# Performance work log

Hardware: AMD Instinct MI355X
Metric: run time of the kernel (lower is better)

The kernel has to match this reference:

```python
import jax, jax.numpy as jnp
import numpy as np

N_NODES = 50000
N_EDGES = 1_600_000
IN_CH = 128
HEADS = 4
OUT_CH = 16
NEG_SLOPE = 0.2


def setup_inputs() -> dict:
    key = jax.random.key(0)
    ks = jax.random.split(key, 6)
    x = jax.random.normal(ks[0], (N_NODES, IN_CH), dtype=jnp.float32)
    row = jax.random.randint(ks[1], (N_EDGES,), 0, N_NODES, dtype=jnp.int32)
    # offset in [1, N) guarantees no self loops in the input graph
    off = jax.random.randint(ks[2], (N_EDGES,), 1, N_NODES, dtype=jnp.int32)
    col = (row + off) % N_NODES
    edge_index = jnp.stack([row, col], axis=0)  # [2, E]
    edge_attr = jax.random.uniform(ks[3], (N_EDGES, HEADS), dtype=jnp.float32)
    weight = jax.random.normal(ks[4], (IN_CH, HEADS * OUT_CH), dtype=jnp.float32) * (1.0 / np.sqrt(IN_CH))
    att_weight = jax.random.normal(ks[5], (1, HEADS, 2 * OUT_CH), dtype=jnp.float32) * 0.1
    bias = jnp.zeros((HEADS * OUT_CH,), dtype=jnp.float32)
    return {"x": x, "edge_index": edge_index, "edge_attr": edge_attr,
            "weight": weight, "att_weight": att_weight, "bias": bias}


def reference(x, edge_index, edge_attr, weight, att_weight, bias):
    N = x.shape[0]
    H, C = HEADS, OUT_CH
    # linear projection: [N, in] @ [in, H*C] -> [N, H, C]
    h = (x @ weight).reshape(N, H, C)
    # add self loops (input is guaranteed self-loop free); self-loop edge_attr = 1
    loop = jnp.arange(N, dtype=edge_index.dtype)
    row = jnp.concatenate([edge_index[0], loop])
    col = jnp.concatenate([edge_index[1], loop])
    ea = jnp.concatenate([edge_attr, jnp.ones((N, H), dtype=edge_attr.dtype)], axis=0)
    edge_index_full = jnp.stack([row, col], axis=0)
    # attention score: cat([h[row], h[col]], -1) * att_weight, summed over feature dim
    a_src = att_weight[0, :, :C]   # [H, C]
    a_dst = att_weight[0, :, C:]   # [H, C]
    alpha = (jnp.einsum('ehc,hc->eh', h[row], a_src)
             + jnp.einsum('ehc,hc->eh', h[col], a_dst))  # [E+N, H]
    alpha = jnp.where(alpha >= 0, alpha, NEG_SLOPE * alpha)  # leaky_relu
    alpha = alpha * ea
    # weighted aggregation: scatter-add messages to row nodes
    msg = alpha[:, :, None] * h[col]                 # [E+N, H, C]
    out = jax.ops.segment_sum(msg, row, num_segments=N)  # [N, H, C]
    out = out.reshape(N, H * C) + bias               # concat heads
    return (out, edge_index_full, alpha)
```

## Files before the change

### kernel.cpp

```cpp
#include <hip/hip_runtime.h>

#define N_NODES 50000
#define N_EDGES 1600000
#define IN_CH 128
#define HEADS 4
#define HC 64
#define E_FULL (N_EDGES + N_NODES)
#define NEG_SLOPE 0.2f

#define BUCKET_NODES 98
#define NBUCK 512
#define BIN_TILE 2048
#define NBLK_BIN ((N_EDGES + BIN_TILE - 1) / BIN_TILE)
#define T_FLAT (NBUCK * NBLK_BIN)
#define SCANA_BLOCKS (T_FLAT / 256)

typedef __attribute__((ext_vector_type(8))) short short8v;
typedef __attribute__((ext_vector_type(4))) float float4v;

__device__ __forceinline__ float leaky(float s) { return s >= 0.f ? s : NEG_SLOPE * s; }

__device__ __forceinline__ unsigned f2bf(float f) {
    unsigned u = __float_as_uint(f);
    return (u + 0x7fffu + ((u >> 16) & 1u)) >> 16;
}
__device__ __forceinline__ float bf2f(unsigned v) {
    return __uint_as_float(v << 16);
}

__global__ __launch_bounds__(256) void wcvt_kernel(
    const float* __restrict__ w, unsigned short* __restrict__ wT)
{
    int i = blockIdx.x * 256 + threadIdx.x;
    if (i < IN_CH * HC) {
        int k = i >> 6, c = i & 63;
        wT[c * IN_CH + k] = (unsigned short)f2bf(w[i]);
    }
}

__global__ __launch_bounds__(256) void gemm_h_kernel(
    const float* __restrict__ x, const unsigned short* __restrict__ wT,
    const float* __restrict__ att, unsigned short* __restrict__ h16,
    float* __restrict__ s_src, float* __restrict__ s_dst)
{
    __shared__ unsigned short x_lds[64 * 128];
    const int tid = threadIdx.x;
    const int nbase = blockIdx.x * 64;

    #pragma unroll
    for (int s = 0; s < 8; ++s) {
        int i = s * 256 + tid;
        int node = i >> 5;
        int q = i & 31;
        float4 v = make_float4(0.f, 0.f, 0.f, 0.f);
        int gn = nbase + node;
        if (gn < N_NODES) v = ((const float4*)x)[(size_t)gn * 32 + q];
        ushort4 b;
        b.x = (unsigned short)f2bf(v.x);
        b.y = (unsigned short)f2bf(v.y);
        b.z = (unsigned short)f2bf(v.z);
        b.w = (unsigned short)f2bf(v.w);
        int chunk = q >> 1, half = q & 1;
        int sw = chunk ^ (node & 7);
        *(ushort4*)&x_lds[node * 128 + sw * 8 + half * 4] = b;
    }
    __syncthreads();

    const int wid = tid >> 6, lane = tid & 63;
    const int g = lane >> 4, m = lane & 15;
    const int rt = wid;

    float4v acc[4] = {{0.f,0.f,0.f,0.f},{0.f,0.f,0.f,0.f},
                      {0.f,0.f,0.f,0.f},{0.f,0.f,0.f,0.f}};
    #pragma unroll
    for (int kk = 0; kk < 4; ++kk) {
        int chunk = (kk * 4 + g) ^ (m & 7);
        short8v a = *(const short8v*)&x_lds[(rt * 16 + m) * 128 + chunk * 8];
        #pragma unroll
        for (int ct = 0; ct < 4; ++ct) {
            short8v bfr = *(const short8v*)&wT[(ct * 16 + m) * IN_CH + kk * 32 + g * 8];
            acc[ct] = __builtin_amdgcn_mfma_f32_16x16x32_bf16(a, bfr, acc[ct], 0, 0, 0);
        }
    }

    #pragma unroll
    for (int ct = 0; ct < 4; ++ct) {
        float as = att[ct * 32 + m];
        float ad = att[ct * 32 + 16 + m];
        float ts[4], td[4];
        #pragma unroll
        for (int r = 0; r < 4; ++r) {
            int node = nbase + rt * 16 + g * 4 + r;
            float v = acc[ct][r];
            if (node < N_NODES)
                h16[(size_t)node * HC + ct * 16 + m] = (unsigned short)f2bf(v);
            ts[r] = v * as;
            td[r] = v * ad;
        }
        #pragma unroll
        for (int msk = 1; msk <= 8; msk <<= 1) {
            #pragma unroll
            for (int r = 0; r < 4; ++r) {
                ts[r] += __shfl_xor(ts[r], msk, 64);
                td[r] += __shfl_xor(td[r], msk, 64);
            }
        }
        if (m == 0) {
            #pragma unroll
            for (int r = 0; r < 4; ++r) {
                int node = nbase + rt * 16 + g * 4 + r;
                if (node < N_NODES) {
                    s_src[node * HEADS + ct] = ts[r];
                    s_dst[node * HEADS + ct] = td[r];
                }
            }
        }
    }
}

__global__ __launch_bounds__(256) void histM_kernel(
    const int* __restrict__ ei, unsigned* __restrict__ M,
    float* __restrict__ eif)
{
    __shared__ unsigned lh[NBUCK];
    const int tid = threadIdx.x;
    for (int j = tid; j < NBUCK; j += 256) lh[j] = 0;
    __syncthreads();
    const int base = blockIdx.x * BIN_TILE;
    #pragma unroll
    for (int k = 0; k < 8; ++k) {
        int e = base + k * 256 + tid;
        if (e < N_EDGES) {
            unsigned r = (unsigned)ei[e];
            unsigned c = (unsigned)ei[N_EDGES + e];
            eif[e] = (float)r;
            eif[(size_t)E_FULL + e] = (float)c;
            atomicAdd(&lh[r / BUCKET_NODES], 1u);
        }
    }
    __syncthreads();
    unsigned* Mb = M + (size_t)blockIdx.x * NBUCK;
    for (int j = tid; j < NBUCK; j += 256) Mb[j] = lh[j];
}

__device__ __forceinline__ unsigned block_excl_scan(unsigned v, unsigned* total,
                                                    int tid) {
    const int lane = tid & 63, wid = tid >> 6;
    unsigned x = v;
    #pragma unroll
    for (int d = 1; d < 64; d <<= 1) {
        unsigned t = __shfl_up(x, d, 64);
        if (lane >= d) x += t;
    }
    __shared__ unsigned wsum[4];
    if (lane == 63) wsum[wid] = x;
    __syncthreads();
    unsigned woff = 0;
    for (int i = 0; i < wid; ++i) woff += wsum[i];
    unsigned incl = x + woff;
    if (tid == 255) *total = incl;
    return incl - v;
}

__global__ __launch_bounds__(256) void scanA_kernel(
    const unsigned* __restrict__ M, unsigned* __restrict__ localx,
    unsigned* __restrict__ partials)
{
    const int tid = threadIdx.x;
    const int f = blockIdx.x * 256 + tid;
    unsigned v = 0;
    if (f < T_FLAT) {
        int bucket = f / NBLK_BIN;
        int blk = f - bucket * NBLK_BIN;
        v = M[(size_t)blk * NBUCK + bucket];
    }
    __shared__ unsigned tot;
    unsigned excl = block_excl_scan(v, &tot, tid);
    if (f < T_FLAT) localx[f] = excl;
    __syncthreads();
    if (tid == 0) partials[blockIdx.x] = tot;
}

__global__ __launch_bounds__(256) void scanB_kernel(
    const unsigned* __restrict__ partials, unsigned* __restrict__ pscan)
{
    __shared__ unsigned tot_sh;
    __shared__ unsigned carry_sh;
    const int tid = threadIdx.x;
    if (tid == 0) carry_sh = 0;
    __syncthreads();
    const int nchunk = (SCANA_BLOCKS + 255) / 256;
    for (int ch = 0; ch < nchunk; ++ch) {
        int i = ch * 256 + tid;
        unsigned v = (i < SCANA_BLOCKS) ? partials[i] : 0u;
        unsigned excl = block_excl_scan(v, &tot_sh, tid);
        unsigned carry = carry_sh;
        if (i < SCANA_BLOCKS) pscan[i] = excl + carry;
        __syncthreads();
        if (tid == 0) carry_sh += tot_sh;
        __syncthreads();
    }
}

__global__ __launch_bounds__(256) void scanC_kernel(
    const unsigned* __restrict__ localx, const unsigned* __restrict__ pscan,
    unsigned* __restrict__ S)
{
    const int f = blockIdx.x * 256 + threadIdx.x;
    if (f < T_FLAT) S[f] = localx[f] + pscan[blockIdx.x];
    if (f == 0) S[T_FLAT] = N_EDGES;
}

__global__ __launch_bounds__(256) void bin_kernel(
    const int* __restrict__ ei, const float* __restrict__ ea,
    const float* __restrict__ s_src, const float* __restrict__ s_dst,
    const unsigned* __restrict__ S, uint4* __restrict__ slots,
    float* __restrict__ alpha)
{
    __shared__ unsigned lh[NBUCK];
    __shared__ unsigned lbase[NBUCK];
    const int tid = threadIdx.x;
    for (int j = tid; j < NBUCK; j += 256) lh[j] = 0;
    __syncthreads();

    const int base = blockIdx.x * BIN_TILE;
    unsigned b8[8], idx8[8], p0[8], p1[8], p2[8];
    #pragma unroll
    for (int k = 0; k < 8; ++k) {
        int e = base + k * 256 + tid;
        b8[k] = 0xffffffffu;
        if (e < N_EDGES) {
            unsigned r = (unsigned)ei[e];
            unsigned c = (unsigned)ei[N_EDGES + e];
            float4 ss = ((const float4*)s_src)[r];
            float4 sd = ((const float4*)s_dst)[c];
            float4 eav = ((const float4*)ea)[e];
            float4 a;
            a.x = leaky(ss.x + sd.x) * eav.x;
            a.y = leaky(ss.y + sd.y) * eav.y;
            a.z = leaky(ss.z + sd.z) * eav.z;
            a.w = leaky(ss.w + sd.w) * eav.w;
            ((float4*)alpha)[e] = a;

            unsigned bk = r / BUCKET_NODES;
            unsigned rl = r - bk * BUCKET_NODES;
            b8[k] = bk;
            p0[k] = c | (rl << 16);
            p1[k] = f2bf(a.x) | (f2bf(a.y) << 16);
            p2[k] = f2bf(a.z) | (f2bf(a.w) << 16);
            idx8[k] = atomicAdd(&lh[bk], 1u);
        }
    }
    __syncthreads();
    for (int j = tid; j < NBUCK; j += 256)
        lbase[j] = S[(size_t)j * NBLK_BIN + blockIdx.x];
    __syncthreads();
    #pragma unroll
    for (int k = 0; k < 8; ++k) {
        if (b8[k] != 0xffffffffu)
            slots[lbase[b8[k]] + idx8[k]] = make_uint4(p0[k], p1[k], p2[k], 0u);
    }
}

__global__ __launch_bounds__(256) void sort_kernel(
    const unsigned* __restrict__ S, const uint4* __restrict__ slots,
    uint4* __restrict__ slots2, unsigned* __restrict__ offs)
{
    __shared__ unsigned cnt[BUCKET_NODES];
    __shared__ unsigned cur[BUCKET_NODES];
    const int b = blockIdx.x;
    const int tid = threadIdx.x;
    const unsigned start = S[(size_t)b * NBLK_BIN];
    const unsigned end   = S[(size_t)(b + 1) * NBLK_BIN];

    for (int j = tid; j < BUCKET_NODES; j += 256) cnt[j] = 0;
    __syncthreads();
    for (unsigned i = start + tid; i < end; i += 256)
        atomicAdd(&cnt[slots[i].x >> 16], 1u);
    __syncthreads();
    if (tid == 0) {
        unsigned run = 0;
        for (int j = 0; j < BUCKET_NODES; ++j) {
            unsigned c = cnt[j];
            cur[j] = run;
            run += c;
        }
    }
    __syncthreads();
    const int nstart = b * BUCKET_NODES;
    for (int j = tid; j < BUCKET_NODES; j += 256) {
        int n = nstart + j;
        if (n <= N_NODES) offs[n] = start + cur[j];
    }
    __syncthreads();
    for (unsigned i = start + tid; i < end; i += 256) {
        uint4 s = slots[i];
        unsigned rl = s.x >> 16;
        unsigned pos = start + atomicAdd(&cur[rl], 1u);
        slots2[pos] = s;
    }
}

__device__ __forceinline__ float slot_alpha(uint4 s, int hd) {
    unsigned w = (hd & 2) ? s.z : s.y;
    return bf2f((hd & 1) ? (w >> 16) : (w & 0xffffu));
}

__global__ __launch_bounds__(256) void gather_kernel(
    const unsigned short* __restrict__ h16, const float* __restrict__ s_src,
    const float* __restrict__ s_dst, const float* __restrict__ bias,
    const unsigned* __restrict__ offs, const uint4* __restrict__ slots2,
    float* __restrict__ alpha, float* __restrict__ out, float* __restrict__ eif)
{
    const int tid = threadIdx.x;
    const int n = blockIdx.x * 4 + (tid >> 6);
    if (n >= N_NODES) return;
    const int lane = tid & 63, hd = lane >> 4;

    float s_self = s_src[n * HEADS + hd] + s_dst[n * HEADS + hd];
    float acc = bias[lane] + leaky(s_self) * bf2f(h16[(size_t)n * HC + lane]);

    const unsigned start = offs[n];
    const int cnt = (int)(offs[n + 1] - start);

    int i = 0;
    for (; i + 7 < cnt; i += 8) {
        uint4 sl[8];
        float hv[8];
        #pragma unroll
        for (int u = 0; u < 8; ++u) sl[u] = slots2[start + i + u];
        #pragma unroll
        for (int u = 0; u < 8; ++u)
            hv[u] = bf2f(h16[(size_t)(sl[u].x & 0xffffu) * HC + lane]);
        #pragma unroll
        for (int u = 0; u < 8; ++u)
            acc = fmaf(slot_alpha(sl[u], hd), hv[u], acc);
    }
    for (; i < cnt; ++i) {
        uint4 s0 = slots2[start + i];
        float h0 = bf2f(h16[(size_t)(s0.x & 0xffffu) * HC + lane]);
        acc = fmaf(slot_alpha(s0, hd), h0, acc);
    }
    out[(size_t)n * HC + lane] = acc;

    if (lane < HEADS) {
        float s2 = s_src[n * HEADS + lane] + s_dst[n * HEADS + lane];
        alpha[(size_t)(N_EDGES + n) * HEADS + lane] = leaky(s2);
    }
    if (lane == 4) eif[N_EDGES + n] = (float)n;
    if (lane == 5) eif[(size_t)E_FULL + N_EDGES + n] = (float)n;
}

extern "C" void kernel_launch(void* const* d_in, const int* in_sizes, int n_in,
                              void* d_out, int out_size, void* d_ws, size_t ws_size,
                              hipStream_t stream) {
    const float* x      = (const float*)d_in[0];
    const int*   ei     = (const int*)  d_in[1];
    const float* ea     = (const float*)d_in[2];
    const float* weight = (const float*)d_in[3];
    const float* att    = (const float*)d_in[4];
    const float* bias   = (const float*)d_in[5];

    float* out   = (float*)d_out;
    float* eif   = out + (size_t)N_NODES * HC;
    float* alpha = eif + (size_t)2 * E_FULL;

    uint4* slots  = (uint4*)d_ws;
    uint4* slots2 = slots + (size_t)N_EDGES;
    unsigned short* wT = (unsigned short*)(slots2 + (size_t)N_EDGES);
    unsigned short* h16 = wT + (size_t)IN_CH * HC;
    float* s_src = (float*)(h16 + (size_t)N_NODES * HC);
    float* s_dst = s_src + (size_t)N_NODES * HEADS;
    unsigned* M        = (unsigned*)(s_dst + (size_t)N_NODES * HEADS);
    unsigned* localx   = M + (size_t)NBLK_BIN * NBUCK;
    unsigned* partials = localx + T_FLAT;
    unsigned* pscan    = partials + SCANA_BLOCKS;
    unsigned* S        = pscan + SCANA_BLOCKS;
    unsigned* offs     = S + (T_FLAT + 1);

    wcvt_kernel<<<(IN_CH * HC + 255) / 256, 256, 0, stream>>>(weight, wT);
    gemm_h_kernel<<<(N_NODES + 63) / 64, 256, 0, stream>>>(x, wT, att, h16, s_src, s_dst);
    histM_kernel<<<NBLK_BIN, 256, 0, stream>>>(ei, M, eif);
    scanA_kernel<<<SCANA_BLOCKS, 256, 0, stream>>>(M, localx, partials);
    scanB_kernel<<<1, 256, 0, stream>>>(partials, pscan);
    scanC_kernel<<<SCANA_BLOCKS, 256, 0, stream>>>(localx, pscan, S);
    bin_kernel<<<NBLK_BIN, 256, 0, stream>>>(ei, ea, s_src, s_dst, S, slots, alpha);
    sort_kernel<<<NBUCK, 256, 0, stream>>>(S, slots, slots2, offs);
    gather_kernel<<<(N_NODES + 3) / 4, 256, 0, stream>>>(
        h16, s_src, s_dst, bias, offs, slots2, alpha, out, eif);
}
```

Before: 167.5 us.

## Fuse edge histogram into GEMM and replace multi-pass scan with atomic bucket cursors

Folds the per-block bucket histogram into the GEMM kernel, which runs with the same grid size. Each block now atomically adds its local counts into a global 512-entry bucket count instead of writing a per-block count matrix. The three-kernel scan over that matrix becomes one 512-thread scan, and bin_kernel reserves space in each bucket with global atomicAdd on a cursor. This cuts launches and the count-matrix traffic, but the order of edges within a bucket now depends on block scheduling, so floating-point summation order is no longer deterministic.

Result: slower. 180.3 us (+7.7%).

```diff
diff --git a/kernel.cpp b/kernel.cpp
--- a/kernel.cpp
+++ b/kernel.cpp
@@ -12,8 +12,6 @@
 #define NBUCK 512
 #define BIN_TILE 2048
 #define NBLK_BIN ((N_EDGES + BIN_TILE - 1) / BIN_TILE)
-#define T_FLAT (NBUCK * NBLK_BIN)
-#define SCANA_BLOCKS (T_FLAT / 256)
 
 typedef __attribute__((ext_vector_type(8))) short short8v;
 typedef __attribute__((ext_vector_type(4))) float float4v;
@@ -38,14 +36,19 @@
     }
 }
 
-__global__ __launch_bounds__(256) void gemm_h_kernel(
+__global__ __launch_bounds__(256) void gemm_hist_kernel(
     const float* __restrict__ x, const unsigned short* __restrict__ wT,
-    const float* __restrict__ att, unsigned short* __restrict__ h16,
-    float* __restrict__ s_src, float* __restrict__ s_dst)
+    const float* __restrict__ att, const int* __restrict__ ei,
+    unsigned short* __restrict__ h16,
+    float* __restrict__ s_src, float* __restrict__ s_dst,
+    unsigned* __restrict__ bucket_cnt, float* __restrict__ eif)
 {
     __shared__ unsigned short x_lds[64 * 128];
+    __shared__ unsigned lh[NBUCK];
     const int tid = threadIdx.x;
     const int nbase = blockIdx.x * 64;
+
+    for (int j = tid; j < NBUCK; j += 256) lh[j] = 0;
 
     #pragma unroll
     for (int s = 0; s < 8; ++s) {
@@ -116,20 +119,11 @@
             }
         }
     }
-}
-
-__global__ __launch_bounds__(256) void histM_kernel(
-    const int* __restrict__ ei, unsigned* __restrict__ M,
-    float* __restrict__ eif)
-{
-    __shared__ unsigned lh[NBUCK];
-    const int tid = threadIdx.x;
-    for (int j = tid; j < NBUCK; j += 256) lh[j] = 0;
-    __syncthreads();
-    const int base = blockIdx.x * BIN_TILE;
+
+    const int ebase = blockIdx.x * BIN_TILE;
     #pragma unroll
     for (int k = 0; k < 8; ++k) {
-        int e = base + k * 256 + tid;
+        int e = ebase + k * 256 + tid;
         if (e < N_EDGES) {
             unsigned r = (unsigned)ei[e];
             unsigned c = (unsigned)ei[N_EDGES + e];
@@ -139,82 +133,39 @@
         }
     }
     __syncthreads();
-    unsigned* Mb = M + (size_t)blockIdx.x * NBUCK;
-    for (int j = tid; j < NBUCK; j += 256) Mb[j] = lh[j];
-}
-
-__device__ __forceinline__ unsigned block_excl_scan(unsigned v, unsigned* total,
-                                                    int tid) {
+    for (int j = tid; j < NBUCK; j += 256)
+        if (lh[j]) atomicAdd(&bucket_cnt[j], lh[j]);
+}
+
+__global__ __launch_bounds__(512) void scan512_kernel(
+    const unsigned* __restrict__ bucket_cnt, unsigned* __restrict__ base,
+    unsigned* __restrict__ cursor)
+{
+    const int tid = threadIdx.x;
     const int lane = tid & 63, wid = tid >> 6;
+    unsigned v = bucket_cnt[tid];
     unsigned x = v;
     #pragma unroll
     for (int d = 1; d < 64; d <<= 1) {
         unsigned t = __shfl_up(x, d, 64);
         if (lane >= d) x += t;
     }
-    __shared__ unsigned wsum[4];
+    __shared__ unsigned wsum[8];
     if (lane == 63) wsum[wid] = x;
     __syncthreads();
     unsigned woff = 0;
     for (int i = 0; i < wid; ++i) woff += wsum[i];
     unsigned incl = x + woff;
-    if (tid == 255) *total = incl;
-    return incl - v;
-}
-
-__global__ __launch_bounds__(256) void scanA_kernel(
-    const unsigned* __restrict__ M, unsigned* __restrict__ localx,
-    unsigned* __restrict__ partials)
-{
-    const int tid = threadIdx.x;
-    const int f = blockIdx.x * 256 + tid;
-    unsigned v = 0;
-    if (f < T_FLAT) {
-        int bucket = f / NBLK_BIN;
-        int blk = f - bucket * NBLK_BIN;
-        v = M[(size_t)blk * NBUCK + bucket];
-    }
-    __shared__ unsigned tot;
-    unsigned excl = block_excl_scan(v, &tot, tid);
-    if (f < T_FLAT) localx[f] = excl;
-    __syncthreads();
-    if (tid == 0) partials[blockIdx.x] = tot;
-}
-
-__global__ __launch_bounds__(256) void scanB_kernel(
-    const unsigned* __restrict__ partials, unsigned* __restrict__ pscan)
-{
-    __shared__ unsigned tot_sh;
-    __shared__ unsigned carry_sh;
-    const int tid = threadIdx.x;
-    if (tid == 0) carry_sh = 0;
-    __syncthreads();
-    const int nchunk = (SCANA_BLOCKS + 255) / 256;
-    for (int ch = 0; ch < nchunk; ++ch) {
-        int i = ch * 256 + tid;
-        unsigned v = (i < SCANA_BLOCKS) ? partials[i] : 0u;
-        unsigned excl = block_excl_scan(v, &tot_sh, tid);
-        unsigned carry = carry_sh;
-        if (i < SCANA_BLOCKS) pscan[i] = excl + carry;
-        __syncthreads();
-        if (tid == 0) carry_sh += tot_sh;
-        __syncthreads();
-    }
-}
-
-__global__ __launch_bounds__(256) void scanC_kernel(
-    const unsigned* __restrict__ localx, const unsigned* __restrict__ pscan,
-    unsigned* __restrict__ S)
-{
-    const int f = blockIdx.x * 256 + threadIdx.x;
-    if (f < T_FLAT) S[f] = localx[f] + pscan[blockIdx.x];
-    if (f == 0) S[T_FLAT] = N_EDGES;
+    unsigned excl = incl - v;
+    base[tid] = excl;
+    cursor[tid] = excl;
+    if (tid == 511) base[512] = incl;
 }
 
 __global__ __launch_bounds__(256) void bin_kernel(
     const int* __restrict__ ei, const float* __restrict__ ea,
     const float* __restrict__ s_src, const float* __restrict__ s_dst,
-    const unsigned* __restrict__ S, uint4* __restrict__ slots,
+    unsigned* __restrict__ cursor, uint4* __restrict__ slots,
     float* __restrict__ alpha)
 {
     __shared__ unsigned lh[NBUCK];
@@ -223,11 +174,11 @@
     for (int j = tid; j < NBUCK; j += 256) lh[j] = 0;
     __syncthreads();
 
-    const int base = blockIdx.x * BIN_TILE;
+    const int ebase = blockIdx.x * BIN_TILE;
     unsigned b8[8], idx8[8], p0[8], p1[8], p2[8];
     #pragma unroll
     for (int k = 0; k < 8; ++k) {
-        int e = base + k * 256 + tid;
+        int e = ebase + k * 256 + tid;
         b8[k] = 0xffffffffu;
         if (e < N_EDGES) {
             unsigned r = (unsigned)ei[e];
@@ -253,7 +204,7 @@
     }
     __syncthreads();
     for (int j = tid; j < NBUCK; j += 256)
-        lbase[j] = S[(size_t)j * NBLK_BIN + blockIdx.x];
+        if (lh[j]) lbase[j] = atomicAdd(&cursor[j], lh[j]);
     __syncthreads();
     #pragma unroll
     for (int k = 0; k < 8; ++k) {
@@ -263,15 +214,15 @@
 }
 
 __global__ __launch_bounds__(256) void sort_kernel(
-    const unsigned* __restrict__ S, const uint4* __restrict__ slots,
+    const unsigned* __restrict__ base, const uint4* __restrict__ slots,
     uint4* __restrict__ slots2, unsigned* __restrict__ offs)
 {
     __shared__ unsigned cnt[BUCKET_NODES];
     __shared__ unsigned cur[BUCKET_NODES];
     const int b = blockIdx.x;
     const int tid = threadIdx.x;
-    const unsigned start = S[(size_t)b * NBLK_BIN];
-    const unsigned end   = S[(size_t)(b + 1) * NBLK_BIN];
+    const unsigned start = base[b];
+    const unsigned end   = base[b + 1];
 
     for (int j = tid; j < BUCKET_NODES; j += 256) cnt[j] = 0;
     __syncthreads();
@@ -371,21 +322,19 @@
     unsigned short* h16 = wT + (size_t)IN_CH * HC;
     float* s_src = (float*)(h16 + (size_t)N_NODES * HC);
     float* s_dst = s_src + (size_t)N_NODES * HEADS;
-    unsigned* M        = (unsigned*)(s_dst + (size_t)N_NODES * HEADS);
-    unsigned* localx   = M + (size_t)NBLK_BIN * NBUCK;
-    unsigned* partials = localx + T_FLAT;
-    unsigned* pscan    = partials + SCANA_BLOCKS;
-    unsigned* S        = pscan + SCANA_BLOCKS;
-    unsigned* offs     = S + (T_FLAT + 1);
+    unsigned* bucket_cnt = (unsigned*)(s_dst + (size_t)N_NODES * HEADS);
+    unsigned* base       = bucket_cnt + NBUCK;
+    unsigned* cursor     = base + (NBUCK + 1);
+    unsigned* offs       = cursor + NBUCK;
+
+    (void)hipMemsetAsync(bucket_cnt, 0, NBUCK * sizeof(unsigned), stream);
 
     wcvt_kernel<<<(IN_CH * HC + 255) / 256, 256, 0, stream>>>(weight, wT);
-    gemm_h_kernel<<<(N_NODES + 63) / 64, 256, 0, stream>>>(x, wT, att, h16, s_src, s_dst);
-    histM_kernel<<<NBLK_BIN, 256, 0, stream>>>(ei, M, eif);
-    scanA_kernel<<<SCANA_BLOCKS, 256, 0, stream>>>(M, localx, partials);
-    scanB_kernel<<<1, 256, 0, stream>>>(partials, pscan);
-    scanC_kernel<<<SCANA_BLOCKS, 256, 0, stream>>>(localx, pscan, S);
-    bin_kernel<<<NBLK_BIN, 256, 0, stream>>>(ei, ea, s_src, s_dst, S, slots, alpha);
-    sort_kernel<<<NBUCK, 256, 0, stream>>>(S, slots, slots2, offs);
+    gemm_hist_kernel<<<NBLK_BIN, 256, 0, stream>>>(
+        x, wT, att, ei, h16, s_src, s_dst, bucket_cnt, eif);
+    scan512_kernel<<<1, 512, 0, stream>>>(bucket_cnt, base, cursor);
+    bin_kernel<<<NBLK_BIN, 256, 0, stream>>>(ei, ea, s_src, s_dst, cursor, slots, alpha);
+    sort_kernel<<<NBUCK, 256, 0, stream>>>(base, slots, slots2, offs);
     gather_kernel<<<(N_NODES + 3) / 4, 256, 0, stream>>>(
         h16, s_src, s_dst, bias, offs, slots2, alpha, out, eif);
 }
```

## Split 16-byte edge slots into meta and alpha arrays, move eif writes into binning

Applied to the files above, without the earlier changes.

The padded uint4 edge slot (with an unused fourth word) becomes two structure-of-arrays buffers: a 4-byte meta word and an 8-byte packed bf16 alpha pair. This cuts slot traffic in the bin, sort and gather kernels from 16 to 12 bytes per edge. The float edge-index output writes move from the histogram kernel into the bin kernel, so the histogram pass only reads the row indices. The gather kernel uses nontemporal loads and stores for the streamed slots and the output. The cost is two separate scattered stores per edge instead of one, and more work in the bin kernel.

Result: slower. 205.5 us (+22.7%).

```diff
diff --git a/kernel.cpp b/kernel.cpp
--- a/kernel.cpp
+++ b/kernel.cpp
@@ -119,8 +119,7 @@
 }
 
 __global__ __launch_bounds__(256) void histM_kernel(
-    const int* __restrict__ ei, unsigned* __restrict__ M,
-    float* __restrict__ eif)
+    const int* __restrict__ ei, unsigned* __restrict__ M)
 {
     __shared__ unsigned lh[NBUCK];
     const int tid = threadIdx.x;
@@ -130,13 +129,8 @@
     #pragma unroll
     for (int k = 0; k < 8; ++k) {
         int e = base + k * 256 + tid;
-        if (e < N_EDGES) {
-            unsigned r = (unsigned)ei[e];
-            unsigned c = (unsigned)ei[N_EDGES + e];
-            eif[e] = (float)r;
-            eif[(size_t)E_FULL + e] = (float)c;
-            atomicAdd(&lh[r / BUCKET_NODES], 1u);
-        }
+        if (e < N_EDGES)
+            atomicAdd(&lh[(unsigned)ei[e] / BUCKET_NODES], 1u);
     }
     __syncthreads();
     unsigned* Mb = M + (size_t)blockIdx.x * NBUCK;
@@ -214,8 +208,8 @@
 __global__ __launch_bounds__(256) void bin_kernel(
     const int* __restrict__ ei, const float* __restrict__ ea,
     const float* __restrict__ s_src, const float* __restrict__ s_dst,
-    const unsigned* __restrict__ S, uint4* __restrict__ slots,
-    float* __restrict__ alpha)
+    const unsigned* __restrict__ S, unsigned* __restrict__ meta,
+    uint2* __restrict__ ab, float* __restrict__ alpha, float* __restrict__ eif)
 {
     __shared__ unsigned lh[NBUCK];
     __shared__ unsigned lbase[NBUCK];
@@ -241,6 +235,8 @@
             a.z = leaky(ss.z + sd.z) * eav.z;
             a.w = leaky(ss.w + sd.w) * eav.w;
             ((float4*)alpha)[e] = a;
+            eif[e] = (float)r;
+            eif[(size_t)E_FULL + e] = (float)c;
 
             unsigned bk = r / BUCKET_NODES;
             unsigned rl = r - bk * BUCKET_NODES;
@@ -257,14 +253,18 @@
     __syncthreads();
     #pragma unroll
     for (int k = 0; k < 8; ++k) {
-        if (b8[k] != 0xffffffffu)
-            slots[lbase[b8[k]] + idx8[k]] = make_uint4(p0[k], p1[k], p2[k], 0u);
+        if (b8[k] != 0xffffffffu) {
+            unsigned pos = lbase[b8[k]] + idx8[k];
+            meta[pos] = p0[k];
+            ab[pos] = make_uint2(p1[k], p2[k]);
+        }
     }
 }
 
 __global__ __launch_bounds__(256) void sort_kernel(
-    const unsigned* __restrict__ S, const uint4* __restrict__ slots,
-    uint4* __restrict__ slots2, unsigned* __restrict__ offs)
+    const unsigned* __restrict__ S, const unsigned* __restrict__ meta,
+    const uint2* __restrict__ ab, unsigned* __restrict__ meta2,
+    uint2* __restrict__ ab2, unsigned* __restrict__ offs)
 {
     __shared__ unsigned cnt[BUCKET_NODES];
     __shared__ unsigned cur[BUCKET_NODES];
@@ -276,7 +276,7 @@
     for (int j = tid; j < BUCKET_NODES; j += 256) cnt[j] = 0;
     __syncthreads();
     for (unsigned i = start + tid; i < end; i += 256)
-        atomicAdd(&cnt[slots[i].x >> 16], 1u);
+        atomicAdd(&cnt[meta[i] >> 16], 1u);
     __syncthreads();
     if (tid == 0) {
         unsigned run = 0;
@@ -294,23 +294,21 @@
     }
     __syncthreads();
     for (unsigned i = start + tid; i < end; i += 256) {
-        uint4 s = slots[i];
-        unsigned rl = s.x >> 16;
+        unsigned m = meta[i];
+        uint2 v = ab[i];
+        unsigned rl = m >> 16;
         unsigned pos = start + atomicAdd(&cur[rl], 1u);
-        slots2[pos] = s;
-    }
-}
-
-__device__ __forceinline__ float slot_alpha(uint4 s, int hd) {
-    unsigned w = (hd & 2) ? s.z : s.y;
-    return bf2f((hd & 1) ? (w >> 16) : (w & 0xffffu));
+        meta2[pos] = m;
+        ab2[pos] = v;
+    }
 }
 
 __global__ __launch_bounds__(256) void gather_kernel(
     const unsigned short* __restrict__ h16, const float* __restrict__ s_src,
     const float* __restrict__ s_dst, const float* __restrict__ bias,
-    const unsigned* __restrict__ offs, const uint4* __restrict__ slots2,
-    float* __restrict__ alpha, float* __restrict__ out, float* __restrict__ eif)
+    const unsigned* __restrict__ offs, const unsigned* __restrict__ meta2,
+    const uint2* __restrict__ ab2, float* __restrict__ alpha,
+    float* __restrict__ out, float* __restrict__ eif)
 {
     const int tid = threadIdx.x;
     const int n = blockIdx.x * 4 + (tid >> 6);
@@ -325,23 +323,34 @@
 
     int i = 0;
     for (; i + 7 < cnt; i += 8) {
-        uint4 sl[8];
+        unsigned mm[8];
+        unsigned long long vv[8];
         float hv[8];
         #pragma unroll
-        for (int u = 0; u < 8; ++u) sl[u] = slots2[start + i + u];
+        for (int u = 0; u < 8; ++u) {
+            mm[u] = __builtin_nontemporal_load(&meta2[start + i + u]);
+            vv[u] = __builtin_nontemporal_load(
+                (const unsigned long long*)&ab2[start + i + u]);
+        }
         #pragma unroll
         for (int u = 0; u < 8; ++u)
-            hv[u] = bf2f(h16[(size_t)(sl[u].x & 0xffffu) * HC + lane]);
-        #pragma unroll
-        for (int u = 0; u < 8; ++u)
-            acc = fmaf(slot_alpha(sl[u], hd), hv[u], acc);
+            hv[u] = bf2f(h16[(size_t)(mm[u] & 0xffffu) * HC + lane]);
+        #pragma unroll
+        for (int u = 0; u < 8; ++u) {
+            unsigned w = (unsigned)((hd & 2) ? (vv[u] >> 32) : vv[u]);
+            float a = bf2f((hd & 1) ? (w >> 16) : (w & 0xffffu));
+            acc = fmaf(a, hv[u], acc);
+        }
     }
     for (; i < cnt; ++i) {
-        uint4 s0 = slots2[start + i];
-        float h0 = bf2f(h16[(size_t)(s0.x & 0xffffu) * HC + lane]);
-        acc = fmaf(slot_alpha(s0, hd), h0, acc);
-    }
-    out[(size_t)n * HC + lane] = acc;
+        unsigned m = meta2[start + i];
+        unsigned long long v = *(const unsigned long long*)&ab2[start + i];
+        unsigned w = (unsigned)((hd & 2) ? (v >> 32) : v);
+        float a = bf2f((hd & 1) ? (w >> 16) : (w & 0xffffu));
+        float h0 = bf2f(h16[(size_t)(m & 0xffffu) * HC + lane]);
+        acc = fmaf(a, h0, acc);
+    }
+    __builtin_nontemporal_store(acc, &out[(size_t)n * HC + lane]);
 
     if (lane < HEADS) {
         float s2 = s_src[n * HEADS + lane] + s_dst[n * HEADS + lane];
@@ -365,9 +374,11 @@
     float* eif   = out + (size_t)N_NODES * HC;
     float* alpha = eif + (size_t)2 * E_FULL;
 
-    uint4* slots  = (uint4*)d_ws;
-    uint4* slots2 = slots + (size_t)N_EDGES;
-    unsigned short* wT = (unsigned short*)(slots2 + (size_t)N_EDGES);
+    uint2* ab  = (uint2*)d_ws;
+    uint2* ab2 = ab + (size_t)N_EDGES;
+    unsigned* meta  = (unsigned*)(ab2 + (size_t)N_EDGES);
+    unsigned* meta2 = meta + (size_t)N_EDGES;
+    unsigned short* wT = (unsigned short*)(meta2 + (size_t)N_EDGES);
     unsigned short* h16 = wT + (size_t)IN_CH * HC;
     float* s_src = (float*)(h16 + (size_t)N_NODES * HC);
     float* s_dst = s_src + (size_t)N_NODES * HEADS;
@@ -380,12 +391,12 @@
 
     wcvt_kernel<<<(IN_CH * HC + 255) / 256, 256, 0, stream>>>(weight, wT);
     gemm_h_kernel<<<(N_NODES + 63) / 64, 256, 0, stream>>>(x, wT, att, h16, s_src, s_dst);
-    histM_kernel<<<NBLK_BIN, 256, 0, stream>>>(ei, M, eif);
+    histM_kernel<<<NBLK_BIN, 256, 0, stream>>>(ei, M);
     scanA_kernel<<<SCANA_BLOCKS, 256, 0, stream>>>(M, localx, partials);
     scanB_kernel<<<1, 256, 0, stream>>>(partials, pscan);
     scanC_kernel<<<SCANA_BLOCKS, 256, 0, stream>>>(localx, pscan, S);
-    bin_kernel<<<NBLK_BIN, 256, 0, stream>>>(ei, ea, s_src, s_dst, S, slots, alpha);
-    sort_kernel<<<NBUCK, 256, 0, stream>>>(S, slots, slots2, offs);
+    bin_kernel<<<NBLK_BIN, 256, 0, stream>>>(ei, ea, s_src, s_dst, S, meta, ab, alpha, eif);
+    sort_kernel<<<NBUCK, 256, 0, stream>>>(S, meta, ab, meta2, ab2, offs);
     gather_kernel<<<(N_NODES + 3) / 4, 256, 0, stream>>>(
-        h16, s_src, s_dst, bias, offs, slots2, alpha, out, eif);
-}
+        h16, s_src, s_dst, bias, offs, meta2, ab2, alpha, out, eif);
+}
```
